# Performance work log

Measured on AMD Instinct MI355X. Metric: run time of the kernel, lower is better.

The kernel has to match this reference:

```python
import jax, jax.numpy as jnp
import numpy as np

N0, N1, N2, N3 = 8192, 32768, 65536, 65536
CUM = (N0, N0 + N1, N0 + N1 + N2, N0 + N1 + N2 + N3)  # nodes through hop k
NTOT = CUM[3]
EH = (131072, 262144, 262144)                          # edges per hop (per edge type)
ECUM = (EH[0], EH[0] + EH[1], EH[0] + EH[1] + EH[2])
ETOT = ECUM[2]
C, H, T = 64, 256, 3
HH = H // 2
B, L = 16, 512  # N0 == B * L: equal-length note sequences per graph
LN_EPS = 1e-5


def _ln(x, w, b):
    m = x.mean(-1, keepdims=True)
    v = x.var(-1, keepdims=True)
    return (x - m) / jnp.sqrt(v + LN_EPS) * w + b


def _seg_mean(msgs, dst, n):
    s = jax.ops.segment_sum(msgs, dst, num_segments=n)
    cnt = jax.ops.segment_sum(jnp.ones(dst.shape, msgs.dtype), dst, num_segments=n)
    return s / jnp.maximum(cnt, 1.0)[:, None]


def _l2(x):
    return x / jnp.maximum(jnp.linalg.norm(x, axis=-1, keepdims=True), 1e-12)


def _gru_dir(x, wih, whh, bih, bhh, reverse):
    # x: [B, Lt, Din]; torch gate order (r, z, n)
    gi = jnp.einsum('bld,gd->blg', x, wih) + bih
    gi = jnp.moveaxis(gi, 1, 0)  # [Lt, B, 3*HH]
    h0 = jnp.zeros((x.shape[0], HH), x.dtype)

    def step(h, g):
        gh = h @ whh.T + bhh
        ir, iz, in_ = jnp.split(g, 3, -1)
        hr, hz, hn = jnp.split(gh, 3, -1)
        r = jax.nn.sigmoid(ir + hr)
        z = jax.nn.sigmoid(iz + hz)
        n = jnp.tanh(in_ + r * hn)
        hnew = (1.0 - z) * n + z * h
        return hnew, hnew

    _, ys = jax.lax.scan(step, h0, gi, reverse=reverse)
    return jnp.moveaxis(ys, 0, 1)  # [B, Lt, HH]


def _bigru(x, wih, whh, bih, bhh):
    f = _gru_dir(x, wih[0], whh[0], bih[0], bhh[0], False)
    bwd = _gru_dir(x, wih[1], whh[1], bih[1], bhh[1], True)
    return jnp.concatenate([f, bwd], -1)


def _forward(x, edge_index, batch_size, sage0_proj_w, sage0_proj_b, sage0_lw, sage0_lb,
             sage0_rw, sage_lw, sage_lb, sage_rw, ln_w, ln_b,
             gru_wih0, gru_whh0, gru_bih0, gru_bhh0,
             gru_wih1, gru_whh1, gru_bih1, gru_bhh1,
             rnn_norm_w, rnn_norm_b, mlp1_w, mlp1_b, mlp_ln_w, mlp_ln_b,
             mlp2_w, mlp2_b, cat_w, cat_b):
    # ---- hybrid GRU branch on seed notes (equal lengths -> pad == reshape) ----
    xs = x[:batch_size].reshape(B, L, C)
    h = _bigru(xs, gru_wih0, gru_whh0, gru_bih0, gru_bhh0)
    h = _bigru(h, gru_wih1, gru_whh1, gru_bih1, gru_bhh1)  # inter-layer dropout: eval mode
    h = _ln(h, rnn_norm_w, rnn_norm_b)
    h = _ln(jax.nn.relu(h @ mlp1_w + mlp1_b), mlp_ln_w, mlp_ln_b) @ mlp2_w + mlp2_b
    x_rnn = h.reshape(batch_size, H)

    # ---- GNN layer 0: SAGEConv(project=True, normalize=True), hetero mean over T types ----
    feat = x
    outs = []
    for t in range(T):
        src, dst = edge_index[t, 0], edge_index[t, 1]
        xp = jax.nn.relu(feat @ sage0_proj_w[t] + sage0_proj_b[t])
        agg = _seg_mean(xp[src], dst, NTOT)
        outs.append(_l2(agg @ sage0_lw[t] + sage0_lb[t] + feat @ sage0_rw[t]))
    feat = sum(outs) / T
    feat = _ln(jax.nn.relu(feat), ln_w[0], ln_b[0])  # dropout: eval mode (identity)

    # ---- layers 1..2 with trim_to_layer: drop last sampled hop each layer ----
    n_layer = (CUM[2], CUM[1])
    e_layer = (ECUM[1], ECUM[0])
    for i in range(2):
        n, e = n_layer[i], e_layer[i]
        feat = feat[:n]
        outs = []
        for t in range(T):
            src, dst = edge_index[t, 0, :e], edge_index[t, 1, :e]
            agg = _seg_mean(feat[src], dst, n)
            outs.append(agg @ sage_lw[i, t] + sage_lb[i, t] + feat @ sage_rw[i, t])
        feat = sum(outs) / T
        if i == 0:
            feat = _ln(jax.nn.relu(feat), ln_w[1], ln_b[1])
    x_gnn = feat[:batch_size]
    return jnp.concatenate([x_rnn, x_gnn], -1) @ cat_w + cat_b


def setup_inputs():
    key = jax.random.key(0)
    ks = iter(jax.random.split(key, 64))

    def nrm(shape, fan_in):
        return jax.random.normal(next(ks), shape, jnp.float32) / float(np.sqrt(fan_in))

    # hop-structured edges: hop k has src < CUM[k+1], dst < CUM[k]
    ei = []
    for t in range(T):
        rows, cols = [], []
        for k in range(3):
            rows.append(jax.random.randint(next(ks), (EH[k],), 0, CUM[k + 1]))
            cols.append(jax.random.randint(next(ks), (EH[k],), 0, CUM[k]))
        ei.append(jnp.stack([jnp.concatenate(rows), jnp.concatenate(cols)]))
    edge_index = jnp.stack(ei).astype(jnp.int32)

    return dict(
        x=jax.random.normal(next(ks), (NTOT, C), jnp.float32),
        edge_index=edge_index,
        batch=(jnp.arange(N0) // L).astype(jnp.int32),
        batch_size=N0,
        sage0_proj_w=nrm((T, C, C), C), sage0_proj_b=jnp.zeros((T, C), jnp.float32),
        sage0_lw=nrm((T, C, H), C), sage0_lb=jnp.zeros((T, H), jnp.float32),
        sage0_rw=nrm((T, C, H), C),
        sage_lw=nrm((2, T, H, H), H), sage_lb=jnp.zeros((2, T, H), jnp.float32),
        sage_rw=nrm((2, T, H, H), H),
        ln_w=jnp.ones((2, H), jnp.float32), ln_b=jnp.zeros((2, H), jnp.float32),
        gru_wih0=nrm((2, 3 * HH, C), C), gru_whh0=nrm((2, 3 * HH, HH), HH),
        gru_bih0=jnp.zeros((2, 3 * HH), jnp.float32), gru_bhh0=jnp.zeros((2, 3 * HH), jnp.float32),
        gru_wih1=nrm((2, 3 * HH, H), H), gru_whh1=nrm((2, 3 * HH, HH), HH),
        gru_bih1=jnp.zeros((2, 3 * HH), jnp.float32), gru_bhh1=jnp.zeros((2, 3 * HH), jnp.float32),
        rnn_norm_w=jnp.ones((H,), jnp.float32), rnn_norm_b=jnp.zeros((H,), jnp.float32),
        mlp1_w=nrm((H, H), H), mlp1_b=jnp.zeros((H,), jnp.float32),
        mlp_ln_w=jnp.ones((H,), jnp.float32), mlp_ln_b=jnp.zeros((H,), jnp.float32),
        mlp2_w=nrm((H, H), H), mlp2_b=jnp.zeros((H,), jnp.float32),
        cat_w=nrm((2 * H, H), 2 * H), cat_b=jnp.zeros((H,), jnp.float32),
    )


def reference(x, edge_index, batch, batch_size, sage0_proj_w, sage0_proj_b, sage0_lw,
              sage0_lb, sage0_rw, sage_lw, sage_lb, sage_rw, ln_w, ln_b,
              gru_wih0, gru_whh0, gru_bih0, gru_bhh0, gru_wih1, gru_whh1, gru_bih1,
              gru_bhh1, rnn_norm_w, rnn_norm_b, mlp1_w, mlp1_b, mlp_ln_w, mlp_ln_b,
              mlp2_w, mlp2_b, cat_w, cat_b):
    # batch encodes 16 equal-length (512) sequences; bincount/pad == reshape above
    return _forward(x, edge_index, batch_size, sage0_proj_w, sage0_proj_b, sage0_lw,
                    sage0_lb, sage0_rw, sage_lw, sage_lb, sage_rw, ln_w, ln_b,
                    gru_wih0, gru_whh0, gru_bih0, gru_bhh0, gru_wih1, gru_whh1,
                    gru_bih1, gru_bhh1, rnn_norm_w, rnn_norm_b, mlp1_w, mlp1_b,
                    mlp_ln_w, mlp_ln_b, mlp2_w, mlp2_b, cat_w, cat_b)
```

## Files before the change

### kernel.cpp

```cpp
#include <hip/hip_runtime.h>
#include <stdint.h>

typedef unsigned short u16;
typedef __attribute__((ext_vector_type(8))) short short8;
typedef __attribute__((ext_vector_type(4))) short short4v;
typedef __attribute__((ext_vector_type(4))) float float4v;

#define DEV static __device__ __forceinline__

DEV float bf2f(u16 u){ union { unsigned int i; float f; } c; c.i = ((unsigned int)u) << 16; return c.f; }
DEV u16 f2bf(float f){ union { float ff; unsigned int i; } c; c.ff = f;
  unsigned int x = c.i; return (u16)((x + 0x7fffu + ((x >> 16) & 1u)) >> 16); }

#define MFMA16(a,b,c) __builtin_amdgcn_mfma_f32_16x16x32_bf16((a),(b),(c),0,0,0)

#define ETOTC  655360
#define TSTRIDE 155648
#define NBINS   466944

__global__ void detect_dtype(const u16* __restrict__ xs, int* __restrict__ flag){
  __shared__ int sh[256];
  int t = threadIdx.x; int cnt = 0;
  for (int i = t; i < 4096; i += 256){
    u16 u = xs[i]; int e = (u >> 7) & 0xff;
    cnt += (u == 0 || (e >= 112 && e <= 143)) ? 1 : 0;
  }
  sh[t] = cnt; __syncthreads();
  for (int d = 128; d; d >>= 1){ if (t < d) sh[t] += sh[t+d]; __syncthreads(); }
  if (t == 0) flag[0] = (sh[0] >= 3686) ? 1 : 0;
}

DEV u16 scrub(u16 v){ int e = (v >> 7) & 0xff; return (e == 0xff) ? (u16)0 : v; }

__global__ void convert_x(const void* __restrict__ xin, const int* __restrict__ flag,
                          u16* __restrict__ out){
  int i = blockIdx.x*256 + threadIdx.x;
  u16 v[4];
  if (flag[0] == 1){
    short4v s = ((const short4v*)xin)[i];
#pragma unroll
    for (int j=0;j<4;j++) v[j] = scrub((u16)s[j]);
  } else {
    float4v f = ((const float4v*)xin)[i];
#pragma unroll
    for (int j=0;j<4;j++) v[j] = scrub(f2bf(f[j]));
  }
  short4v o; o[0]=(short)v[0]; o[1]=(short)v[1]; o[2]=(short)v[2]; o[3]=(short)v[3];
  ((short4v*)out)[i] = o;
}

struct WSrc { const void* p[28]; };
__device__ const int g_wcum[29] = {0,12288,12480,61632,62400,111552,504768,506304,899520,
  900032,900544,949696,1048000,1048768,1049536,1246144,1344448,1345216,1345984,1346240,
  1346496,1412032,1412288,1412544,1412800,1478336,1478592,1609664,1609920};

__global__ void convert_w(WSrc d, const int* __restrict__ flag, u16* __restrict__ out){
  int i = blockIdx.x*256 + threadIdx.x;
  if (i >= 1609920) return;
  int lo = 0, hi = 28;
  while (hi - lo > 1){ int m = (lo+hi) >> 1; if (i >= g_wcum[m]) lo = m; else hi = m; }
  int off = i - g_wcum[lo];
  u16 v = (flag[0] == 1) ? ((const u16*)d.p[lo])[off]
                         : f2bf(((const float*)d.p[lo])[off]);
  out[i] = scrub(v);
}

__global__ void packT(const u16* __restrict__ in, u16* __restrict__ out, int K, int N){
  int i = blockIdx.x*256 + threadIdx.x;
  if (i < K*N){ int n = i / K, k = i - n*K; out[i] = in[(size_t)k*N + n]; }
}

__global__ void pack_lr(const u16* __restrict__ lw, const u16* __restrict__ rw,
                        u16* __restrict__ out, int F){
  int K2 = 2*F; long total = 3L*256*K2;
  long i = (long)blockIdx.x*256 + threadIdx.x;
  if (i < total){
    int k = (int)(i % K2); int n = (int)((i / K2) & 255); int t = (int)(i / ((long)K2*256));
    out[i] = (k < F) ? lw[((size_t)t*F + k)*256 + n]
                     : rw[((size_t)t*F + (k-F))*256 + n];
  }
}

__global__ void hist3(const int* __restrict__ ei, int* __restrict__ cnt){
  int g = blockIdx.x*256 + threadIdx.x;
  int t = g / ETOTC, e = g - t*ETOTC;
  int dst = ei[(size_t)t*2*ETOTC + ETOTC + e];
  int base = t*TSTRIDE;
  atomicAdd(&cnt[base + dst], 1);
  if (e < 393216) atomicAdd(&cnt[base + 106496 + dst], 1);
  if (e < 131072) atomicAdd(&cnt[base + 147456 + dst], 1);
}

__global__ void perm3(const int* __restrict__ ei, const int* __restrict__ off,
                      int* __restrict__ slot, int* __restrict__ srcs){
  int g = blockIdx.x*256 + threadIdx.x;
  int t = g / ETOTC, e = g - t*ETOTC;
  int dst = ei[(size_t)t*2*ETOTC + ETOTC + e];
  int src = ei[(size_t)t*2*ETOTC + e];
  int base = t*TSTRIDE;
  { int b = base + dst; srcs[off[b] + atomicAdd(&slot[b], 1)] = src; }
  if (e < 393216){ int b = base + 106496 + dst;
    srcs[off[b] + atomicAdd(&slot[b], 1)] = src; }
  if (e < 131072){ int b = base + 147456 + dst;
    srcs[off[b] + atomicAdd(&slot[b], 1)] = src; }
}

__global__ void scan_blocks(const int* __restrict__ cnt, int* __restrict__ off,
                            int* __restrict__ bsum, int n){
  __shared__ int sh[256];
  int t = threadIdx.x;
  int base = blockIdx.x*2048 + t*8;
  int v[8]; int tot = 0;
#pragma unroll
  for (int j=0;j<8;j++){ v[j] = (base+j < n) ? cnt[base+j] : 0; tot += v[j]; }
  sh[t] = tot; __syncthreads();
  for (int d=1; d<256; d<<=1){
    int y = (t>=d) ? sh[t-d] : 0; __syncthreads();
    sh[t] += y; __syncthreads();
  }
  int run = sh[t] - tot;
#pragma unroll
  for (int j=0;j<8;j++){ if (base+j < n) off[base+j] = run; run += v[j]; }
  if (t == 255) bsum[blockIdx.x] = sh[255];
}

__global__ void scan_top(int* __restrict__ bsum, int G){
  __shared__ int sh[256];
  int t = threadIdx.x;
  int v = (t < G) ? bsum[t] : 0;
  sh[t] = v; __syncthreads();
  for (int d=1; d<256; d<<=1){
    int y = (t>=d) ? sh[t-d] : 0; __syncthreads();
    sh[t] += y; __syncthreads();
  }
  if (t < G) bsum[t] = sh[t] - v;
}

__global__ void scan_add(int* __restrict__ off, const int* __restrict__ bsum, int n){
  int add = bsum[blockIdx.x];
  int base = blockIdx.x*2048 + threadIdx.x*8;
#pragma unroll
  for (int j=0;j<8;j++) if (base+j < n) off[base+j] += add;
}

template<int F>
__global__ __launch_bounds__(256,4) void gather_mean(
    const int* __restrict__ off, const int* __restrict__ cnt, const int* __restrict__ srcs,
    const u16* __restrict__ feat, int ld, u16* __restrict__ out, int rows)
{
  int w = blockIdx.x*4 + (threadIdx.x >> 6);
  int lane = threadIdx.x & 63;
  if (w >= rows) return;
  int st = off[w], c = cnt[w];
  float sc = 1.f / (float)(c < 1 ? 1 : c);
  if (F == 64) {
    float a = 0.f, b = 0.f;
    int i = 0;
    for (; i + 4 <= c; i += 4){
      int s0 = srcs[st+i], s1 = srcs[st+i+1], s2 = srcs[st+i+2], s3 = srcs[st+i+3];
      u16 u0 = feat[(size_t)s0*ld + lane];
      u16 u1 = feat[(size_t)s1*ld + lane];
      u16 u2 = feat[(size_t)s2*ld + lane];
      u16 u3 = feat[(size_t)s3*ld + lane];
      a += bf2f(u0) + bf2f(u1);
      b += bf2f(u2) + bf2f(u3);
    }
    for (; i < c; ++i){ int s = srcs[st+i]; a += bf2f(feat[(size_t)s*ld + lane]); }
    out[(size_t)w*64 + lane] = f2bf((a + b)*sc);
  } else {
    float a0=0.f,a1=0.f,a2=0.f,a3=0.f;
    float b0=0.f,b1=0.f,b2=0.f,b3=0.f;
    int i = 0;
    for (; i + 4 <= c; i += 4){
      int s0 = srcs[st+i], s1 = srcs[st+i+1], s2 = srcs[st+i+2], s3 = srcs[st+i+3];
      short4v u0 = *(const short4v*)(feat + (size_t)s0*ld + lane*4);
      short4v u1 = *(const short4v*)(feat + (size_t)s1*ld + lane*4);
      short4v u2 = *(const short4v*)(feat + (size_t)s2*ld + lane*4);
      short4v u3 = *(const short4v*)(feat + (size_t)s3*ld + lane*4);
      a0 += bf2f((u16)u0[0]) + bf2f((u16)u1[0]);
      a1 += bf2f((u16)u0[1]) + bf2f((u16)u1[1]);
      a2 += bf2f((u16)u0[2]) + bf2f((u16)u1[2]);
      a3 += bf2f((u16)u0[3]) + bf2f((u16)u1[3]);
      b0 += bf2f((u16)u2[0]) + bf2f((u16)u3[0]);
      b1 += bf2f((u16)u2[1]) + bf2f((u16)u3[1]);
      b2 += bf2f((u16)u2[2]) + bf2f((u16)u3[2]);
      b3 += bf2f((u16)u2[3]) + bf2f((u16)u3[3]);
    }
    for (; i < c; ++i){
      int s = srcs[st+i];
      short4v u = *(const short4v*)(feat + (size_t)s*ld + lane*4);
      a0 += bf2f((u16)u[0]); a1 += bf2f((u16)u[1]);
      a2 += bf2f((u16)u[2]); a3 += bf2f((u16)u[3]);
    }
    u16* o = out + (size_t)w*256 + lane*4;
    o[0]=f2bf((a0+b0)*sc); o[1]=f2bf((a1+b1)*sc);
    o[2]=f2bf((a2+b2)*sc); o[3]=f2bf((a3+b3)*sc);
  }
}

__global__ __launch_bounds__(256,2) void ln_rows(
    const u16* __restrict__ in, u16* __restrict__ out,
    const u16* __restrict__ w, const u16* __restrict__ b, int rows)
{
  int r = blockIdx.x*4 + (threadIdx.x >> 6);
  int lane = threadIdx.x & 63;
  if (r >= rows) return;
  short4v u = *(const short4v*)(in + (size_t)r*256 + lane*4);
  float v[4];
#pragma unroll
  for (int i=0;i<4;i++) v[i] = bf2f((u16)u[i]);
  float s = v[0]+v[1]+v[2]+v[3];
  float q = v[0]*v[0]+v[1]*v[1]+v[2]*v[2]+v[3]*v[3];
#pragma unroll
  for (int d=1; d<64; d<<=1){ s += __shfl_xor(s, d); q += __shfl_xor(q, d); }
  float mu = s * (1.f/256.f);
  float var = fmaxf(q * (1.f/256.f) - mu*mu, 0.f);
  float rs = rsqrtf(var + 1e-5f);
  u16* o = out + (size_t)r*256 + lane*4;
#pragma unroll
  for (int i=0;i<4;i++){
    int col = lane*4 + i;
    o[i] = f2bf((v[i]-mu)*rs*bf2f(w[col]) + bf2f(b[col]));
  }
}

#define LGKM0_SB do{ asm volatile("s_waitcnt lgkmcnt(0)" ::: "memory"); \
                     __builtin_amdgcn_sched_barrier(0); \
                     __builtin_amdgcn_s_barrier(); \
                     __builtin_amdgcn_sched_barrier(0); }while(0)

#define GRU_STEP(S, C0, C1, C2) do{                                          \
    const int l_ = dir ? (511 - (S)) : (S);                                  \
    short8 afr_[4];                                                          \
    _Pragma("unroll")                                                        \
    for (int kt=0; kt<4; kt++) afr_[kt] = *(const short8*)(&hbf[kt*32 + lg*8]); \
    float4v acc_[4];                                                         \
    _Pragma("unroll")                                                        \
    for (int nt=0; nt<4; nt++) acc_[nt] = (float4v){0.f,0.f,0.f,0.f};        \
    _Pragma("unroll")                                                        \
    for (int kt=0; kt<4; kt++){                                              \
      _Pragma("unroll")                                                      \
      for (int nt=0; nt<4; nt++) acc_[nt] = MFMA16(afr_[kt], bfrag[nt][kt], acc_[nt]); } \
    if (lane < 16){                                                          \
      _Pragma("unroll")                                                      \
      for (int nt=0; nt<4; nt++) ghs[64*w + nt*16 + lane] = acc_[nt][0];     \
    }                                                                        \
    LGKM0_SB;                                                                \
    if (tid < 128){                                                          \
      float ghr = ghs[tid]       + bhr;                                      \
      float ghz = ghs[128 + tid] + bhz;                                      \
      float ghn = ghs[256 + tid] + bhn;                                      \
      float r_ = 1.f/(1.f + __expf(-((C0) + ghr)));                          \
      float z_ = 1.f/(1.f + __expf(-((C1) + ghz)));                          \
      float xn_ = (C2) + r_*ghn;                                             \
      float th_ = 1.f - 2.f/(__expf(2.f*xn_) + 1.f);                         \
      hreg = (1.f - z_)*th_ + z_*hreg;                                       \
      u16 hb_ = f2bf(hreg);                                                  \
      hbf[tid] = hb_;                                                        \
      hout[((size_t)(b*512 + l_))*256 + dir*128 + tid] = hb_;                \
      int sn_ = (S) + 2;                                                     \
      if (sn_ < 512){                                                        \
        int ln2_ = dir ? (511 - sn_) : sn_;                                  \
        const float* g_ = gbase + (size_t)ln2_*768;                          \
        (C0) = g_[0]; (C1) = g_[128]; (C2) = g_[256];                        \
      }                                                                      \
    }                                                                        \
    LGKM0_SB;                                                                \
  }while(0)

__global__ __launch_bounds__(384,1) void gru_mfma(
    const float* __restrict__ gi, const u16* __restrict__ whh,
    const u16* __restrict__ bhh, u16* __restrict__ hout)
{
  const int b = blockIdx.x >> 1, dir = blockIdx.x & 1;
  const int tid = threadIdx.x;
  const int w = tid >> 6, lane = tid & 63;
  const int lr = lane & 15, lg = lane >> 4;
  __shared__ u16 hbf[128];
  __shared__ float ghs[384];

  short8 bfrag[4][4];
#pragma unroll
  for (int nt=0; nt<4; nt++)
#pragma unroll
    for (int kt=0; kt<4; kt++){
      int n = 64*w + nt*16 + lr;
      bfrag[nt][kt] = *(const short8*)(whh + ((size_t)(dir*384 + n))*128 + kt*32 + lg*8);
    }

  const float* gbase = gi + (size_t)b*512*768 + dir*384 + tid;
  float hreg = 0.f, bhr = 0.f, bhz = 0.f, bhn = 0.f;
  float a0=0.f,a1=0.f,a2=0.f, e0=0.f,e1=0.f,e2=0.f;
  if (tid < 128){
    bhr = bf2f(bhh[dir*384 + tid]);
    bhz = bf2f(bhh[dir*384 + 128 + tid]);
    bhn = bf2f(bhh[dir*384 + 256 + tid]);
    const float* g0 = gbase + (size_t)(dir ? 511 : 0)*768;
    a0 = g0[0]; a1 = g0[128]; a2 = g0[256];
    const float* g1 = gbase + (size_t)(dir ? 510 : 1)*768;
    e0 = g1[0]; e1 = g1[128]; e2 = g1[256];
  }
  if (tid < 64) ((unsigned int*)hbf)[tid] = 0u;
  LGKM0_SB;

  for (int s2 = 0; s2 < 512; s2 += 2){
    GRU_STEP(s2,     a0, a1, a2);
    GRU_STEP(s2 + 1, e0, e1, e2);
  }
}

template<int EPI, bool OUTF32>
__global__ __launch_bounds__(256,1) void gemm_bt(
    const u16* __restrict__ A, int lda,
    const u16* __restrict__ WT, int K, int N,
    const u16* __restrict__ bias,
    const u16* __restrict__ lnw, const u16* __restrict__ lnb,
    void* __restrict__ Cp, int ldc, const int* __restrict__ dynof)
{
  __shared__ u16 As[64*72];
  __shared__ u16 Bs[256*72];
  __shared__ float redS[4][64];
  __shared__ float redQ[4][64];
  __shared__ float muL[64], rsL[64];
  const int tid = threadIdx.x;
  const int lane = tid & 63, wid = tid >> 6;
  const int lr = lane & 15, lg = lane >> 4;
  const int m0 = blockIdx.x * 64;
  const int col0 = blockIdx.y * 256;
  float4v acc[4][4];
#pragma unroll
  for (int i=0;i<4;i++)
#pragma unroll
    for (int j=0;j<4;j++) acc[i][j] = (float4v){0.f,0.f,0.f,0.f};

  for (int k0 = 0; k0 < K; k0 += 64){
#pragma unroll
    for (int v = 0; v < 2; v++){
      int idx = tid + v*256; int r = idx >> 3, c8 = (idx & 7) << 3;
      *(short8*)(&As[r*72 + c8]) = *(const short8*)(A + (size_t)(m0+r)*lda + k0 + c8);
    }
#pragma unroll
    for (int v = 0; v < 8; v++){
      int idx = tid + v*256; int nn = idx >> 3, c8 = (idx & 7) << 3;
      short8 val = {0,0,0,0,0,0,0,0};
      if (col0 + nn < N) val = *(const short8*)(WT + (size_t)(col0+nn)*K + k0 + c8);
      *(short8*)(&Bs[nn*72 + c8]) = val;
    }
    __syncthreads();
#pragma unroll
    for (int kk = 0; kk < 2; kk++){
      short8 af[4], bfr[4];
#pragma unroll
      for (int i=0;i<4;i++) af[i]  = *(const short8*)(&As[(16*i+lr)*72 + kk*32 + lg*8]);
#pragma unroll
      for (int j=0;j<4;j++) bfr[j] = *(const short8*)(&Bs[(wid*64+16*j+lr)*72 + kk*32 + lg*8]);
#pragma unroll
      for (int i=0;i<4;i++)
#pragma unroll
        for (int j=0;j<4;j++) acc[i][j] = MFMA16(af[i], bfr[j], acc[i][j]);
    }
    __syncthreads();
  }
  int cols[4];
#pragma unroll
  for (int j=0;j<4;j++) cols[j] = col0 + wid*64 + 16*j + lr;
#pragma unroll
  for (int j=0;j<4;j++){
    float bv = (cols[j] < N) ? bf2f(bias[cols[j]]) : 0.f;
#pragma unroll
    for (int i=0;i<4;i++)
#pragma unroll
      for (int r=0;r<4;r++) acc[i][j][r] += bv;
  }
  if (EPI >= 1){
#pragma unroll
    for (int i=0;i<4;i++)
#pragma unroll
      for (int j=0;j<4;j++)
#pragma unroll
        for (int r=0;r<4;r++) acc[i][j][r] = fmaxf(acc[i][j][r], 0.f);
  }
  if (EPI == 2){
#pragma unroll
    for (int i=0;i<4;i++)
#pragma unroll
      for (int r=0;r<4;r++){
        float p = acc[i][0][r]+acc[i][1][r]+acc[i][2][r]+acc[i][3][r];
        float q = acc[i][0][r]*acc[i][0][r]+acc[i][1][r]*acc[i][1][r]
                 +acc[i][2][r]*acc[i][2][r]+acc[i][3][r]*acc[i][3][r];
#pragma unroll
        for (int d=1; d<16; d<<=1){ p += __shfl_xor(p,d); q += __shfl_xor(q,d); }
        if (lr == 0){ redS[wid][16*i + lg*4 + r] = p; redQ[wid][16*i + lg*4 + r] = q; }
      }
    __syncthreads();
    if (tid < 64){
      float s = redS[0][tid]+redS[1][tid]+redS[2][tid]+redS[3][tid];
      float q = redQ[0][tid]+redQ[1][tid]+redQ[2][tid]+redQ[3][tid];
      float mu = s * (1.f/256.f);
      float var = fmaxf(q * (1.f/256.f) - mu*mu, 0.f);
      muL[tid] = mu; rsL[tid] = rsqrtf(var + 1e-5f);
    }
    __syncthreads();
#pragma unroll
    for (int i=0;i<4;i++)
#pragma unroll
      for (int r=0;r<4;r++){
        int rl = 16*i + lg*4 + r;
        float mu = muL[rl], rs = rsL[rl];
#pragma unroll
        for (int j=0;j<4;j++){
          float w = bf2f(lnw[cols[j]]), bb = bf2f(lnb[cols[j]]);
          acc[i][j][r] = (acc[i][j][r]-mu)*rs*w + bb;
        }
      }
  }
  bool of32 = OUTF32;
  if (dynof) of32 = (dynof[0] == 0);
#pragma unroll
  for (int i=0;i<4;i++)
#pragma unroll
    for (int r=0;r<4;r++){
      int row = m0 + 16*i + lg*4 + r;
#pragma unroll
      for (int j=0;j<4;j++) if (cols[j] < N){
        if (of32) ((float*)Cp)[(size_t)row*ldc + cols[j]] = acc[i][j][r];
        else ((u16*)Cp)[(size_t)row*ldc + cols[j]] = f2bf(acc[i][j][r]);
      }
    }
}

template<int F, bool DO_L2, bool DO_LN>
__global__ __launch_bounds__(256,1) void sage_fused(
    const u16* __restrict__ A1, long a1t, const u16* __restrict__ A2, int lda2,
    const u16* __restrict__ WTp, const u16* __restrict__ lbp,
    const u16* __restrict__ lnw, const u16* __restrict__ lnb,
    u16* __restrict__ out, int ldc, int outcol)
{
  constexpr int K2 = 2*F;
  __shared__ u16 As[64*72];
  __shared__ u16 Bs[256*72];
  __shared__ float redS[4][64];
  __shared__ float redQ[4][64];
  __shared__ float rowA[64], rowB[64];
  const int tid = threadIdx.x;
  const int lane = tid & 63, wid = tid >> 6;
  const int lr = lane & 15, lg = lane >> 4;
  const int m0 = blockIdx.x * 64;
  int colsL[4];
#pragma unroll
  for (int j=0;j<4;j++) colsL[j] = wid*64 + 16*j + lr;
  float4v facc[4][4];
#pragma unroll
  for (int i=0;i<4;i++)
#pragma unroll
    for (int j=0;j<4;j++) facc[i][j] = (float4v){0.f,0.f,0.f,0.f};

  for (int t=0; t<3; ++t){
    float4v acc[4][4];
#pragma unroll
    for (int i=0;i<4;i++)
#pragma unroll
      for (int j=0;j<4;j++) acc[i][j] = (float4v){0.f,0.f,0.f,0.f};
    const u16* WT  = WTp + (size_t)t*256*K2;
    const u16* A1b = A1 + (size_t)t*a1t;
    for (int k0 = 0; k0 < K2; k0 += 64){
      const u16* Ab; int la, kb;
      if (k0 < F){ Ab = A1b; la = F; kb = k0; } else { Ab = A2; la = lda2; kb = k0 - F; }
#pragma unroll
      for (int v=0; v<2; v++){
        int idx = tid + v*256; int r = idx >> 3, c8 = (idx & 7) << 3;
        *(short8*)(&As[r*72 + c8]) = *(const short8*)(Ab + (size_t)(m0+r)*la + kb + c8);
      }
#pragma unroll
      for (int v=0; v<8; v++){
        int idx = tid + v*256; int nn = idx >> 3, c8 = (idx & 7) << 3;
        *(short8*)(&Bs[nn*72 + c8]) = *(const short8*)(WT + (size_t)nn*K2 + k0 + c8);
      }
      __syncthreads();
#pragma unroll
      for (int kk = 0; kk < 2; kk++){
        short8 af[4], bfr[4];
#pragma unroll
        for (int i=0;i<4;i++) af[i]  = *(const short8*)(&As[(16*i+lr)*72 + kk*32 + lg*8]);
#pragma unroll
        for (int j=0;j<4;j++) bfr[j] = *(const short8*)(&Bs[(wid*64+16*j+lr)*72 + kk*32 + lg*8]);
#pragma unroll
        for (int i=0;i<4;i++)
#pragma unroll
          for (int j=0;j<4;j++) acc[i][j] = MFMA16(af[i], bfr[j], acc[i][j]);
      }
      __syncthreads();
    }
#pragma unroll
    for (int j=0;j<4;j++){
      float bv = bf2f(lbp[t*256 + colsL[j]]);
#pragma unroll
      for (int i=0;i<4;i++)
#pragma unroll
        for (int r=0;r<4;r++) acc[i][j][r] += bv;
    }
    if (DO_L2){
#pragma unroll
      for (int i=0;i<4;i++)
#pragma unroll
        for (int r=0;r<4;r++){
          float q = acc[i][0][r]*acc[i][0][r]+acc[i][1][r]*acc[i][1][r]
                   +acc[i][2][r]*acc[i][2][r]+acc[i][3][r]*acc[i][3][r];
#pragma unroll
          for (int d=1; d<16; d<<=1) q += __shfl_xor(q,d);
          if (lr == 0) redQ[wid][16*i + lg*4 + r] = q;
        }
      __syncthreads();
      if (tid < 64){
        float q = redQ[0][tid]+redQ[1][tid]+redQ[2][tid]+redQ[3][tid];
        rowA[tid] = 1.f / fmaxf(sqrtf(q), 1e-12f);
      }
      __syncthreads();
#pragma unroll
      for (int i=0;i<4;i++)
#pragma unroll
        for (int r=0;r<4;r++){
          float sc = rowA[16*i + lg*4 + r];
#pragma unroll
          for (int j=0;j<4;j++) acc[i][j][r] *= sc;
        }
      __syncthreads();
    }
#pragma unroll
    for (int i=0;i<4;i++)
#pragma unroll
      for (int j=0;j<4;j++)
#pragma unroll
        for (int r=0;r<4;r++) facc[i][j][r] += acc[i][j][r];
  }
  const float inv3 = (1.f/3.f);
#pragma unroll
  for (int i=0;i<4;i++)
#pragma unroll
    for (int j=0;j<4;j++)
#pragma unroll
      for (int r=0;r<4;r++) facc[i][j][r] *= inv3;
  if (DO_LN){
#pragma unroll
    for (int i=0;i<4;i++)
#pragma unroll
      for (int j=0;j<4;j++)
#pragma unroll
        for (int r=0;r<4;r++) facc[i][j][r] = fmaxf(facc[i][j][r], 0.f);
#pragma unroll
    for (int i=0;i<4;i++)
#pragma unroll
      for (int r=0;r<4;r++){
        float p = facc[i][0][r]+facc[i][1][r]+facc[i][2][r]+facc[i][3][r];
        float q = facc[i][0][r]*facc[i][0][r]+facc[i][1][r]*facc[i][1][r]
                 +facc[i][2][r]*facc[i][2][r]+facc[i][3][r]*facc[i][3][r];
#pragma unroll
        for (int d=1; d<16; d<<=1){ p += __shfl_xor(p,d); q += __shfl_xor(q,d); }
        if (lr == 0){ redS[wid][16*i + lg*4 + r] = p; redQ[wid][16*i + lg*4 + r] = q; }
      }
    __syncthreads();
    if (tid < 64){
      float s = redS[0][tid]+redS[1][tid]+redS[2][tid]+redS[3][tid];
      float q = redQ[0][tid]+redQ[1][tid]+redQ[2][tid]+redQ[3][tid];
      float mu = s * (1.f/256.f);
      float var = fmaxf(q * (1.f/256.f) - mu*mu, 0.f);
      rowA[tid] = mu; rowB[tid] = rsqrtf(var + 1e-5f);
    }
    __syncthreads();
#pragma unroll
    for (int i=0;i<4;i++)
#pragma unroll
      for (int r=0;r<4;r++){
        int rl = 16*i + lg*4 + r;
        float mu = rowA[rl], rs = rowB[rl];
#pragma unroll
        for (int j=0;j<4;j++){
          float w = bf2f(lnw[colsL[j]]), bb = bf2f(lnb[colsL[j]]);
          facc[i][j][r] = (facc[i][j][r]-mu)*rs*w + bb;
        }
      }
  }
#pragma unroll
  for (int i=0;i<4;i++)
#pragma unroll
    for (int r=0;r<4;r++){
      int row = m0 + 16*i + lg*4 + r;
#pragma unroll
      for (int j=0;j<4;j++)
        out[(size_t)row*ldc + outcol + colsL[j]] = f2bf(facc[i][j][r]);
    }
}

extern "C" void kernel_launch(void* const* d_in, const int* in_sizes, int n_in,
                              void* d_out, int out_size, void* d_ws, size_t ws_size,
                              hipStream_t stream)
{
  (void)in_sizes; (void)n_in; (void)out_size;
  const int* ei = (const int*)d_in[1];

  char* ws = (char*)d_ws;
  size_t o = 0;
  auto alloc = [&](size_t b){ size_t p = o; o += (b + 255) & ~(size_t)255; return p; };
  char* RA   = ws + alloc(66060288);
  float* GI  = (float*)RA;
  u16* H0    = (u16*)(RA + 25165824);
  u16* H1    = (u16*)(RA + 29360128);
  u16* HA    = (u16*)(RA + 33554432);
  u16* HB    = (u16*)(RA + 37748736);
  u16* XP3   = (u16*)RA;
  u16* AGGB1 = (u16*)RA;
  char* RB   = ws + alloc(40894464);
  u16* AGGB0 = (u16*)RB;
  u16* AGGB2 = (u16*)RB;
  u16* FEAT  = (u16*)(ws + alloc(106496ull*256*2));
  u16* FEAT2 = (u16*)(ws + alloc(40960ull*256*2));
  u16* CAT   = (u16*)(ws + alloc(8192ull*512*2));
  u16* AR    = (u16*)(ws + alloc(12619968ull*2));
  u16* WXP   = (u16*)(ws + alloc(192ull*64*2));
  u16* WP0   = (u16*)(ws + alloc(3ull*256*128*2));
  u16* WP1   = (u16*)(ws + alloc(3ull*256*512*2));
  u16* WP2   = (u16*)(ws + alloc(3ull*256*512*2));
  u16* M1T   = (u16*)(ws + alloc(256ull*256*2));
  u16* M2T   = (u16*)(ws + alloc(256ull*256*2));
  u16* CTT   = (u16*)(ws + alloc(256ull*512*2));
  int* CNT   = (int*)(ws + alloc((size_t)NBINS*4));
  int* OFF   = (int*)(ws + alloc((size_t)NBINS*4));
  int* SLOT  = (int*)(ws + alloc((size_t)NBINS*4));
  int* BSUM  = (int*)(ws + alloc(256ull*4));
  int* SRCS  = (int*)(ws + alloc(3538944ull*4));
  int* FLAG  = (int*)(ws + alloc(256));
  if (o > ws_size) return;

  u16* x16    = AR;
  u16* projw6 = AR + 11010048; u16* projb6 = AR + 11022336;
  u16* s0lw6  = AR + 11022528; u16* s0lb6  = AR + 11071680; u16* s0rw6 = AR + 11072448;
  u16* slw6   = AR + 11121600; u16* slb6   = AR + 11514816; u16* srw6  = AR + 11516352;
  u16* lnw6   = AR + 11909568; u16* lnb6   = AR + 11910080;
  u16* wih0b  = AR + 11910592; u16* whh0b  = AR + 11959744;
  u16* bih0b  = AR + 12058048; u16* bhh0b  = AR + 12058816;
  u16* wih1b  = AR + 12059584; u16* whh1b  = AR + 12256192;
  u16* bih1b  = AR + 12354496; u16* bhh1b  = AR + 12355264;
  u16* rnw6   = AR + 12356032; u16* rnb6   = AR + 12356288;
  u16* mlp1w6 = AR + 12356544; u16* mlp1b6 = AR + 12422080;
  u16* mlnw6  = AR + 12422336; u16* mlnb6  = AR + 12422592;
  u16* mlp2w6 = AR + 12422848; u16* mlp2b6 = AR + 12488384;
  u16* catw6  = AR + 12488640; u16* catb6  = AR + 12619712;

  detect_dtype<<<dim3(1),dim3(256),0,stream>>>((const u16*)d_in[0], FLAG);
  convert_x<<<dim3(10752),dim3(256),0,stream>>>(d_in[0], FLAG, x16);
  WSrc wsrc;
  for (int i=0;i<28;i++) wsrc.p[i] = d_in[4+i];
  convert_w<<<dim3(6289),dim3(256),0,stream>>>(wsrc, FLAG, AR + 11010048);

  packT<<<dim3(256),dim3(256),0,stream>>>(mlp1w6, M1T, 256, 256);
  packT<<<dim3(256),dim3(256),0,stream>>>(mlp2w6, M2T, 256, 256);
  packT<<<dim3(512),dim3(256),0,stream>>>(catw6,  CTT, 512, 256);
  for (int t=0;t<3;t++)
    packT<<<dim3(16),dim3(256),0,stream>>>(projw6 + (size_t)t*4096, WXP + (size_t)t*4096, 64, 64);
  pack_lr<<<dim3(384),dim3(256),0,stream>>>(s0lw6, s0rw6, WP0, 64);
  pack_lr<<<dim3(1536),dim3(256),0,stream>>>(slw6,               srw6,               WP1, 256);
  pack_lr<<<dim3(1536),dim3(256),0,stream>>>(slw6 + 3ull*256*256, srw6 + 3ull*256*256, WP2, 256);

  gemm_bt<0,true><<<dim3(128,3),dim3(256),0,stream>>>(x16, 64, wih0b, 64, 768, bih0b, nullptr, nullptr, GI, 768, nullptr);
  gru_mfma<<<dim3(32),dim3(384),0,stream>>>(GI, whh0b, bhh0b, H0);
  gemm_bt<0,true><<<dim3(128,3),dim3(256),0,stream>>>(H0, 256, wih1b, 256, 768, bih1b, nullptr, nullptr, GI, 768, nullptr);
  gru_mfma<<<dim3(32),dim3(384),0,stream>>>(GI, whh1b, bhh1b, H1);
  ln_rows<<<dim3(2048),dim3(256),0,stream>>>(H1, HA, rnw6, rnb6, 8192);
  gemm_bt<2,false><<<dim3(128,1),dim3(256),0,stream>>>(HA, 256, M1T, 256, 256, mlp1b6, mlnw6, mlnb6, HB, 256, nullptr);
  gemm_bt<0,false><<<dim3(128,1),dim3(256),0,stream>>>(HB, 256, M2T, 256, 256, mlp2b6, nullptr, nullptr, CAT, 512, nullptr);

  hipMemsetAsync(CNT, 0, (size_t)NBINS*4, stream);
  hist3<<<dim3(7680),dim3(256),0,stream>>>(ei, CNT);
  scan_blocks<<<dim3(228),dim3(256),0,stream>>>(CNT, OFF, BSUM, NBINS);
  scan_top<<<dim3(1),dim3(256),0,stream>>>(BSUM, 228);
  scan_add<<<dim3(228),dim3(256),0,stream>>>(OFF, BSUM, NBINS);
  hipMemsetAsync(SLOT, 0, (size_t)NBINS*4, stream);
  perm3<<<dim3(7680),dim3(256),0,stream>>>(ei, OFF, SLOT, SRCS);

  gemm_bt<1,false><<<dim3(2688,1),dim3(256),0,stream>>>(x16, 64, WXP, 64, 192, projb6, nullptr, nullptr, XP3, 192, nullptr);
  for (int t=0;t<3;t++)
    gather_mean<64><<<dim3(26624),dim3(256),0,stream>>>(
        OFF + t*TSTRIDE, CNT + t*TSTRIDE, SRCS, XP3 + t*64, 192,
        AGGB0 + (size_t)t*106496*64, 106496);
  sage_fused<64,true,true><<<dim3(1664),dim3(256),0,stream>>>(
      AGGB0, (long)106496*64, x16, 64, WP0, s0lb6, lnw6, lnb6, FEAT, 256, 0);

  for (int t=0;t<3;t++)
    gather_mean<256><<<dim3(10240),dim3(256),0,stream>>>(
        OFF + t*TSTRIDE + 106496, CNT + t*TSTRIDE + 106496, SRCS, FEAT, 256,
        AGGB1 + (size_t)t*40960*256, 40960);
  sage_fused<256,false,true><<<dim3(640),dim3(256),0,stream>>>(
      AGGB1, (long)40960*256, FEAT, 256, WP1, slb6, lnw6+256, lnb6+256, FEAT2, 256, 0);

  for (int t=0;t<3;t++)
    gather_mean<256><<<dim3(2048),dim3(256),0,stream>>>(
        OFF + t*TSTRIDE + 147456, CNT + t*TSTRIDE + 147456, SRCS, FEAT2, 256,
        AGGB2 + (size_t)t*8192*256, 8192);
  sage_fused<256,false,false><<<dim3(128),dim3(256),0,stream>>>(
      AGGB2, (long)8192*256, FEAT2, 256, WP2, slb6 + 3*256, nullptr, nullptr, CAT, 512, 256);

  gemm_bt<0,false><<<dim3(128,1),dim3(256),0,stream>>>(CAT, 512, CTT, 512, 256, catb6,
      nullptr, nullptr, d_out, 256, FLAG);
}
```

Before: 1.700 ms.

## Restructure GRU recurrence so each wave owns full r/z/n gates, one barrier per step

The GRU recurrent kernel now uses 4 waves (256 threads) instead of 6. Each wave computes the r, z and n gate columns for the same 32 hidden units, so the gate nonlinearity and state update run right in the MFMA lanes without an LDS exchange. A double-buffered hidden-state array replaces the shared gate scratch, which cuts the two block barriers per timestep down to one. The trade-off is more MFMAs and registers per wave and fewer active lanes in the elementwise update.

```diff
diff --git a/kernel.cpp b/kernel.cpp
--- a/kernel.cpp
+++ b/kernel.cpp
@@ -229,46 +229,44 @@
                      __builtin_amdgcn_s_barrier(); \
                      __builtin_amdgcn_sched_barrier(0); }while(0)
 
-#define GRU_STEP(S, C0, C1, C2) do{                                          \
+#define GRU_STEP2(S, RD, WR, Cr0, Cz0, Cn0, Cr1, Cz1, Cn1) do{               \
     const int l_ = dir ? (511 - (S)) : (S);                                  \
     short8 afr_[4];                                                          \
     _Pragma("unroll")                                                        \
-    for (int kt=0; kt<4; kt++) afr_[kt] = *(const short8*)(&hbf[kt*32 + lg*8]); \
-    float4v acc_[4];                                                         \
+    for (int kt=0; kt<4; kt++) afr_[kt] = *(const short8*)(&hbf2[RD][kt*32 + lg*8]); \
+    float4v acc_[6];                                                         \
     _Pragma("unroll")                                                        \
-    for (int nt=0; nt<4; nt++) acc_[nt] = (float4v){0.f,0.f,0.f,0.f};        \
+    for (int nt=0; nt<6; nt++) acc_[nt] = (float4v){0.f,0.f,0.f,0.f};        \
     _Pragma("unroll")                                                        \
     for (int kt=0; kt<4; kt++){                                              \
       _Pragma("unroll")                                                      \
-      for (int nt=0; nt<4; nt++) acc_[nt] = MFMA16(afr_[kt], bfrag[nt][kt], acc_[nt]); } \
+      for (int nt=0; nt<6; nt++) acc_[nt] = MFMA16(afr_[kt], bfrag[nt][kt], acc_[nt]); } \
     if (lane < 16){                                                          \
-      _Pragma("unroll")                                                      \
-      for (int nt=0; nt<4; nt++) ghs[64*w + nt*16 + lane] = acc_[nt][0];     \
-    }                                                                        \
-    LGKM0_SB;                                                                \
-    if (tid < 128){                                                          \
-      float ghr = ghs[tid]       + bhr;                                      \
-      float ghz = ghs[128 + tid] + bhz;                                      \
-      float ghn = ghs[256 + tid] + bhn;                                      \
-      float r_ = 1.f/(1.f + __expf(-((C0) + ghr)));                          \
-      float z_ = 1.f/(1.f + __expf(-((C1) + ghz)));                          \
-      float xn_ = (C2) + r_*ghn;                                             \
-      float th_ = 1.f - 2.f/(__expf(2.f*xn_) + 1.f);                         \
-      hreg = (1.f - z_)*th_ + z_*hreg;                                       \
-      u16 hb_ = f2bf(hreg);                                                  \
-      hbf[tid] = hb_;                                                        \
-      hout[((size_t)(b*512 + l_))*256 + dir*128 + tid] = hb_;                \
+      float r0_ = 1.f/(1.f + __expf(-((Cr0) + acc_[0][0] + bh0)));           \
+      float r1_ = 1.f/(1.f + __expf(-((Cr1) + acc_[1][0] + bh1)));           \
+      float z0_ = 1.f/(1.f + __expf(-((Cz0) + acc_[2][0] + bh2)));           \
+      float z1_ = 1.f/(1.f + __expf(-((Cz1) + acc_[3][0] + bh3)));           \
+      float xn0_ = (Cn0) + r0_*(acc_[4][0] + bh4);                           \
+      float xn1_ = (Cn1) + r1_*(acc_[5][0] + bh5);                           \
+      float th0_ = 1.f - 2.f/(__expf(2.f*xn0_) + 1.f);                       \
+      float th1_ = 1.f - 2.f/(__expf(2.f*xn1_) + 1.f);                       \
+      hreg0 = (1.f - z0_)*th0_ + z0_*hreg0;                                  \
+      hreg1 = (1.f - z1_)*th1_ + z1_*hreg1;                                  \
+      u16 hb0_ = f2bf(hreg0), hb1_ = f2bf(hreg1);                            \
+      hbf2[WR][hi0] = hb0_; hbf2[WR][hi1] = hb1_;                            \
+      u16* op_ = hout + ((size_t)(b*512 + l_))*256 + dir*128;                \
+      op_[hi0] = hb0_; op_[hi1] = hb1_;                                      \
       int sn_ = (S) + 2;                                                     \
       if (sn_ < 512){                                                        \
-        int ln2_ = dir ? (511 - sn_) : sn_;                                  \
-        const float* g_ = gbase + (size_t)ln2_*768;                          \
-        (C0) = g_[0]; (C1) = g_[128]; (C2) = g_[256];                        \
+        const float* g_ = gptr + (size_t)(dir ? (511 - sn_) : sn_)*768;      \
+        (Cr0)=g_[hi0]; (Cz0)=g_[128+hi0]; (Cn0)=g_[256+hi0];                 \
+        (Cr1)=g_[hi1]; (Cz1)=g_[128+hi1]; (Cn1)=g_[256+hi1];                 \
       }                                                                      \
     }                                                                        \
     LGKM0_SB;                                                                \
   }while(0)
 
-__global__ __launch_bounds__(384,1) void gru_mfma(
+__global__ __launch_bounds__(256,1) void gru_mfma(
     const float* __restrict__ gi, const u16* __restrict__ whh,
     const u16* __restrict__ bhh, u16* __restrict__ hout)
 {
@@ -276,36 +274,39 @@
   const int tid = threadIdx.x;
   const int w = tid >> 6, lane = tid & 63;
   const int lr = lane & 15, lg = lane >> 4;
-  __shared__ u16 hbf[128];
-  __shared__ float ghs[384];
-
-  short8 bfrag[4][4];
-#pragma unroll
-  for (int nt=0; nt<4; nt++)
+  __shared__ u16 hbf2[2][128];
+
+  short8 bfrag[6][4];
+#pragma unroll
+  for (int nt=0; nt<6; nt++)
 #pragma unroll
     for (int kt=0; kt<4; kt++){
-      int n = 64*w + nt*16 + lr;
+      int n = (nt>>1)*128 + w*32 + (nt&1)*16 + lr;
       bfrag[nt][kt] = *(const short8*)(whh + ((size_t)(dir*384 + n))*128 + kt*32 + lg*8);
     }
 
-  const float* gbase = gi + (size_t)b*512*768 + dir*384 + tid;
-  float hreg = 0.f, bhr = 0.f, bhz = 0.f, bhn = 0.f;
-  float a0=0.f,a1=0.f,a2=0.f, e0=0.f,e1=0.f,e2=0.f;
-  if (tid < 128){
-    bhr = bf2f(bhh[dir*384 + tid]);
-    bhz = bf2f(bhh[dir*384 + 128 + tid]);
-    bhn = bf2f(bhh[dir*384 + 256 + tid]);
-    const float* g0 = gbase + (size_t)(dir ? 511 : 0)*768;
-    a0 = g0[0]; a1 = g0[128]; a2 = g0[256];
-    const float* g1 = gbase + (size_t)(dir ? 510 : 1)*768;
-    e0 = g1[0]; e1 = g1[128]; e2 = g1[256];
-  }
-  if (tid < 64) ((unsigned int*)hbf)[tid] = 0u;
+  const int hi0 = w*32 + lr, hi1 = hi0 + 16;
+  const float* gptr = gi + (size_t)b*512*768 + dir*384;
+  float hreg0 = 0.f, hreg1 = 0.f;
+  float bh0=0,bh1=0,bh2=0,bh3=0,bh4=0,bh5=0;
+  float a0=0,a1=0,a2=0,a3=0,a4=0,a5=0, e0=0,e1=0,e2=0,e3=0,e4=0,e5=0;
+  if (lane < 16){
+    bh0 = bf2f(bhh[dir*384 + hi0]);        bh1 = bf2f(bhh[dir*384 + hi1]);
+    bh2 = bf2f(bhh[dir*384 + 128 + hi0]);  bh3 = bf2f(bhh[dir*384 + 128 + hi1]);
+    bh4 = bf2f(bhh[dir*384 + 256 + hi0]);  bh5 = bf2f(bhh[dir*384 + 256 + hi1]);
+    const float* g0 = gptr + (size_t)(dir ? 511 : 0)*768;
+    a0=g0[hi0]; a1=g0[128+hi0]; a2=g0[256+hi0];
+    a3=g0[hi1]; a4=g0[128+hi1]; a5=g0[256+hi1];
+    const float* g1 = gptr + (size_t)(dir ? 510 : 1)*768;
+    e0=g1[hi0]; e1=g1[128+hi0]; e2=g1[256+hi0];
+    e3=g1[hi1]; e4=g1[128+hi1]; e5=g1[256+hi1];
+  }
+  if (tid < 64) ((unsigned int*)hbf2[0])[tid] = 0u;
   LGKM0_SB;
 
   for (int s2 = 0; s2 < 512; s2 += 2){
-    GRU_STEP(s2,     a0, a1, a2);
-    GRU_STEP(s2 + 1, e0, e1, e2);
+    GRU_STEP2(s2,     0, 1, a0, a1, a2, a3, a4, a5);
+    GRU_STEP2(s2 + 1, 1, 0, e0, e1, e2, e3, e4, e5);
   }
 }
 
@@ -662,9 +663,9 @@
   pack_lr<<<dim3(1536),dim3(256),0,stream>>>(slw6 + 3ull*256*256, srw6 + 3ull*256*256, WP2, 256);
 
   gemm_bt<0,true><<<dim3(128,3),dim3(256),0,stream>>>(x16, 64, wih0b, 64, 768, bih0b, nullptr, nullptr, GI, 768, nullptr);
-  gru_mfma<<<dim3(32),dim3(384),0,stream>>>(GI, whh0b, bhh0b, H0);
+  gru_mfma<<<dim3(32),dim3(256),0,stream>>>(GI, whh0b, bhh0b, H0);
   gemm_bt<0,true><<<dim3(128,3),dim3(256),0,stream>>>(H0, 256, wih1b, 256, 768, bih1b, nullptr, nullptr, GI, 768, nullptr);
-  gru_mfma<<<dim3(32),dim3(384),0,stream>>>(GI, whh1b, bhh1b, H1);
+  gru_mfma<<<dim3(32),dim3(256),0,stream>>>(GI, whh1b, bhh1b, H1);
   ln_rows<<<dim3(2048),dim3(256),0,stream>>>(H1, HA, rnw6, rnb6, 8192);
   gemm_bt<2,false><<<dim3(128,1),dim3(256),0,stream>>>(HA, 256, M1T, 256, 256, mlp1b6, mlnw6, mlnb6, HB, 256, nullptr);
   gemm_bt<0,false><<<dim3(128,1),dim3(256),0,stream>>>(HB, 256, M2T, 256, 256, mlp2b6, nullptr, nullptr, CAT, 512, nullptr);
```

After: 1.749 ms. +2.9%, slower.

## Co-schedule sequential GRU blocks with SAGE neighbor gathers in one launch

Applied to the files above, without the earlier changes.

The GRU recurrence kernels launch only 32 latency-bound blocks, which leaves most of the GPU idle. They are now fused into a single launch with the hop-0 and hop-1 gather_mean work: the first 32 blocks run the GRU and the rest run gathers with 6 waves per block. The workspace is rearranged so the GRU buffers no longer alias the gather buffers, and the GRU-dependent layers move to the end. The risk is that the block scheduler may not start the GRU blocks first, and gather blocks may contend with the GRU for memory bandwidth.

```diff
diff --git a/kernel.cpp b/kernel.cpp
--- a/kernel.cpp
+++ b/kernel.cpp
@@ -144,13 +144,10 @@
 }
 
 template<int F>
-__global__ __launch_bounds__(256,4) void gather_mean(
+DEV void gather_body(int w, int lane,
     const int* __restrict__ off, const int* __restrict__ cnt, const int* __restrict__ srcs,
-    const u16* __restrict__ feat, int ld, u16* __restrict__ out, int rows)
+    const u16* __restrict__ feat, int ld, u16* __restrict__ out)
 {
-  int w = blockIdx.x*4 + (threadIdx.x >> 6);
-  int lane = threadIdx.x & 63;
-  if (w >= rows) return;
   int st = off[w], c = cnt[w];
   float sc = 1.f / (float)(c < 1 ? 1 : c);
   if (F == 64) {
@@ -196,6 +193,17 @@
     o[0]=f2bf((a0+b0)*sc); o[1]=f2bf((a1+b1)*sc);
     o[2]=f2bf((a2+b2)*sc); o[3]=f2bf((a3+b3)*sc);
   }
+}
+
+template<int F>
+__global__ __launch_bounds__(256,4) void gather_mean(
+    const int* __restrict__ off, const int* __restrict__ cnt, const int* __restrict__ srcs,
+    const u16* __restrict__ feat, int ld, u16* __restrict__ out, int rows)
+{
+  int w = blockIdx.x*4 + (threadIdx.x >> 6);
+  int lane = threadIdx.x & 63;
+  if (w >= rows) return;
+  gather_body<F>(w, lane, off, cnt, srcs, feat, ld, out);
 }
 
 __global__ __launch_bounds__(256,2) void ln_rows(
@@ -268,16 +276,14 @@
     LGKM0_SB;                                                                \
   }while(0)
 
-__global__ __launch_bounds__(384,1) void gru_mfma(
-    const float* __restrict__ gi, const u16* __restrict__ whh,
-    const u16* __restrict__ bhh, u16* __restrict__ hout)
+DEV void gru_body(const float* __restrict__ gi, const u16* __restrict__ whh,
+                  const u16* __restrict__ bhh, u16* __restrict__ hout,
+                  int bid, u16* hbf, float* ghs)
 {
-  const int b = blockIdx.x >> 1, dir = blockIdx.x & 1;
+  const int b = bid >> 1, dir = bid & 1;
   const int tid = threadIdx.x;
   const int w = tid >> 6, lane = tid & 63;
   const int lr = lane & 15, lg = lane >> 4;
-  __shared__ u16 hbf[128];
-  __shared__ float ghs[384];
 
   short8 bfrag[4][4];
 #pragma unroll
@@ -307,6 +313,29 @@
     GRU_STEP(s2,     a0, a1, a2);
     GRU_STEP(s2 + 1, e0, e1, e2);
   }
+}
+
+template<int F>
+__global__ __launch_bounds__(384,1) void fused_gru_gather(
+    const float* __restrict__ gi, const u16* __restrict__ whh,
+    const u16* __restrict__ bhh, u16* __restrict__ hout,
+    const int* __restrict__ off0, const int* __restrict__ cnt0, const int* __restrict__ srcs,
+    const u16* __restrict__ feat, int ld, int featstep,
+    u16* __restrict__ aggout, long aggstride, int rows, int bpt)
+{
+  __shared__ u16 hbf[128];
+  __shared__ float ghs[384];
+  if (blockIdx.x < 32){
+    gru_body(gi, whh, bhh, hout, blockIdx.x, hbf, ghs);
+    return;
+  }
+  int gb = blockIdx.x - 32;
+  int t = gb / bpt, rb = gb - t*bpt;
+  int w = rb*6 + (threadIdx.x >> 6);
+  int lane = threadIdx.x & 63;
+  if (w >= rows) return;
+  gather_body<F>(w, lane, off0 + t*TSTRIDE, cnt0 + t*TSTRIDE, srcs,
+                 feat + (size_t)t*featstep, ld, aggout + (size_t)t*aggstride);
 }
 
 template<int EPI, bool OUTF32>
@@ -602,18 +631,19 @@
   size_t o = 0;
   auto alloc = [&](size_t b){ size_t p = o; o += (b + 255) & ~(size_t)255; return p; };
   char* RA   = ws + alloc(66060288);
-  float* GI  = (float*)RA;
-  u16* H0    = (u16*)(RA + 25165824);
-  u16* H1    = (u16*)(RA + 29360128);
-  u16* HA    = (u16*)(RA + 33554432);
-  u16* HB    = (u16*)(RA + 37748736);
   u16* XP3   = (u16*)RA;
   u16* AGGB1 = (u16*)RA;
+  char* RR   = ws + alloc(41943040);
+  float* GI  = (float*)RR;
+  u16* H0    = (u16*)(RR + 25165824);
+  u16* H1    = (u16*)(RR + 29360128);
+  u16* HA    = (u16*)(RR + 33554432);
+  u16* HB    = (u16*)(RR + 37748736);
   char* RB   = ws + alloc(40894464);
   u16* AGGB0 = (u16*)RB;
   u16* AGGB2 = (u16*)RB;
+  u16* FEAT2 = (u16*)(RB + 12582912);
   u16* FEAT  = (u16*)(ws + alloc(106496ull*256*2));
-  u16* FEAT2 = (u16*)(ws + alloc(40960ull*256*2));
   u16* CAT   = (u16*)(ws + alloc(8192ull*512*2));
   u16* AR    = (u16*)(ws + alloc(12619968ull*2));
   u16* WXP   = (u16*)(ws + alloc(192ull*64*2));
@@ -661,14 +691,6 @@
   pack_lr<<<dim3(1536),dim3(256),0,stream>>>(slw6,               srw6,               WP1, 256);
   pack_lr<<<dim3(1536),dim3(256),0,stream>>>(slw6 + 3ull*256*256, srw6 + 3ull*256*256, WP2, 256);
 
-  gemm_bt<0,true><<<dim3(128,3),dim3(256),0,stream>>>(x16, 64, wih0b, 64, 768, bih0b, nullptr, nullptr, GI, 768, nullptr);
-  gru_mfma<<<dim3(32),dim3(384),0,stream>>>(GI, whh0b, bhh0b, H0);
-  gemm_bt<0,true><<<dim3(128,3),dim3(256),0,stream>>>(H0, 256, wih1b, 256, 768, bih1b, nullptr, nullptr, GI, 768, nullptr);
-  gru_mfma<<<dim3(32),dim3(384),0,stream>>>(GI, whh1b, bhh1b, H1);
-  ln_rows<<<dim3(2048),dim3(256),0,stream>>>(H1, HA, rnw6, rnb6, 8192);
-  gemm_bt<2,false><<<dim3(128,1),dim3(256),0,stream>>>(HA, 256, M1T, 256, 256, mlp1b6, mlnw6, mlnb6, HB, 256, nullptr);
-  gemm_bt<0,false><<<dim3(128,1),dim3(256),0,stream>>>(HB, 256, M2T, 256, 256, mlp2b6, nullptr, nullptr, CAT, 512, nullptr);
-
   hipMemsetAsync(CNT, 0, (size_t)NBINS*4, stream);
   hist3<<<dim3(7680),dim3(256),0,stream>>>(ei, CNT);
   scan_blocks<<<dim3(228),dim3(256),0,stream>>>(CNT, OFF, BSUM, NBINS);
@@ -677,21 +699,23 @@
   hipMemsetAsync(SLOT, 0, (size_t)NBINS*4, stream);
   perm3<<<dim3(7680),dim3(256),0,stream>>>(ei, OFF, SLOT, SRCS);
 
+  gemm_bt<0,true><<<dim3(128,3),dim3(256),0,stream>>>(x16, 64, wih0b, 64, 768, bih0b, nullptr, nullptr, GI, 768, nullptr);
   gemm_bt<1,false><<<dim3(2688,1),dim3(256),0,stream>>>(x16, 64, WXP, 64, 192, projb6, nullptr, nullptr, XP3, 192, nullptr);
-  for (int t=0;t<3;t++)
-    gather_mean<64><<<dim3(26624),dim3(256),0,stream>>>(
-        OFF + t*TSTRIDE, CNT + t*TSTRIDE, SRCS, XP3 + t*64, 192,
-        AGGB0 + (size_t)t*106496*64, 106496);
+
+  fused_gru_gather<64><<<dim3(32 + 3*17750),dim3(384),0,stream>>>(
+      GI, whh0b, bhh0b, H0,
+      OFF, CNT, SRCS, XP3, 192, 64, AGGB0, (long)106496*64, 106496, 17750);
+
+  gemm_bt<0,true><<<dim3(128,3),dim3(256),0,stream>>>(H0, 256, wih1b, 256, 768, bih1b, nullptr, nullptr, GI, 768, nullptr);
   sage_fused<64,true,true><<<dim3(1664),dim3(256),0,stream>>>(
       AGGB0, (long)106496*64, x16, 64, WP0, s0lb6, lnw6, lnb6, FEAT, 256, 0);
 
-  for (int t=0;t<3;t++)
-    gather_mean<256><<<dim3(10240),dim3(256),0,stream>>>(
-        OFF + t*TSTRIDE + 106496, CNT + t*TSTRIDE + 106496, SRCS, FEAT, 256,
-        AGGB1 + (size_t)t*40960*256, 40960);
+  fused_gru_gather<256><<<dim3(32 + 3*6827),dim3(384),0,stream>>>(
+      GI, whh1b, bhh1b, H1,
+      OFF + 106496, CNT + 106496, SRCS, FEAT, 256, 0, AGGB1, (long)40960*256, 40960, 6827);
+
   sage_fused<256,false,true><<<dim3(640),dim3(256),0,stream>>>(
       AGGB1, (long)40960*256, FEAT, 256, WP1, slb6, lnw6+256, lnb6+256, FEAT2, 256, 0);
-
   for (int t=0;t<3;t++)
     gather_mean<256><<<dim3(2048),dim3(256),0,stream>>>(
         OFF + t*TSTRIDE + 147456, CNT + t*TSTRIDE + 147456, SRCS, FEAT2, 256,
@@ -699,6 +723,10 @@
   sage_fused<256,false,false><<<dim3(128),dim3(256),0,stream>>>(
       AGGB2, (long)8192*256, FEAT2, 256, WP2, slb6 + 3*256, nullptr, nullptr, CAT, 512, 256);
 
+  ln_rows<<<dim3(2048),dim3(256),0,stream>>>(H1, HA, rnw6, rnb6, 8192);
+  gemm_bt<2,false><<<dim3(128,1),dim3(256),0,stream>>>(HA, 256, M1T, 256, 256, mlp1b6, mlnw6, mlnb6, HB, 256, nullptr);
+  gemm_bt<0,false><<<dim3(128,1),dim3(256),0,stream>>>(HB, 256, M2T, 256, 256, mlp2b6, nullptr, nullptr, CAT, 512, nullptr);
+
   gemm_bt<0,false><<<dim3(128,1),dim3(256),0,stream>>>(CAT, 512, CTT, 512, 256, catb6,
       nullptr, nullptr, d_out, 256, FLAG);
 }
```

Measured after the change: 1.526 ms. 1.11x faster.
